# Optimization experiments

Hardware: AMD Instinct MI355X
Metric: run time of the kernel (lower is better)

The kernel has to match this reference:

```python
import jax, jax.numpy as jnp
import numpy as np


def setup_inputs() -> dict:
    key = jax.random.key(0)
    ks = jax.random.split(key, 5)
    B, Cin, Ch, H, W, K = 8, 64, 64, 128, 128, 3
    fan_in = (Cin + Ch) * K * K
    return {
        "x": jax.random.normal(ks[0], (B, Cin, H, W), jnp.float32),
        "prev_h": jax.random.normal(ks[1], (B, Ch, H, W), jnp.float32),
        "prev_c": jax.random.normal(ks[2], (B, Ch, H, W), jnp.float32),
        "W_gates": jax.random.normal(ks[3], (4 * Ch, Cin + Ch, K, K), jnp.float32) / np.sqrt(fan_in),
        "b_gates": jax.random.normal(ks[4], (4 * Ch,), jnp.float32) * 0.01,
    }


def reference(x, prev_h, prev_c, W_gates, b_gates):
    # ConvLSTM cell: conv over concat(input, prev_h) -> 4 gates -> gating.
    pad = W_gates.shape[-1] // 2
    stacked = jnp.concatenate([x, prev_h], axis=1)  # [B, Cin+Ch, H, W]
    gates = jax.lax.conv_general_dilated(
        stacked, W_gates,
        window_strides=(1, 1),
        padding=[(pad, pad), (pad, pad)],
        dimension_numbers=("NCHW", "OIHW", "NCHW"),
    ) + b_gates[None, :, None, None]  # [B, 4*Ch, H, W]
    in_gate, remember_gate, out_gate, cell_gate = jnp.split(gates, 4, axis=1)
    in_gate = jax.nn.sigmoid(in_gate)
    remember_gate = jax.nn.sigmoid(remember_gate)
    out_gate = jax.nn.sigmoid(out_gate)
    cell_gate = jnp.tanh(cell_gate)
    cell = in_gate * cell_gate + remember_gate * prev_c
    hidden = out_gate * jnp.tanh(cell)
    return (hidden, cell)
```

## Files before the change

### kernel.cpp

```cpp
#include <hip/hip_runtime.h>

typedef __attribute__((ext_vector_type(8))) short short8;
typedef __attribute__((ext_vector_type(4))) float float4v;

#define NPIX_HID 8388608
#define PST 136

__device__ __forceinline__ short f2bf(float f) {
    union { float f; unsigned u; } v; v.f = f;
    unsigned r = (v.u + 0x7FFFu + ((v.u >> 16) & 1u)) >> 16;
    return (short)r;
}

__device__ __forceinline__ float sigmoidf_(float v) { return 1.f / (1.f + __expf(-v)); }
__device__ __forceinline__ float tanhf_(float v)    { return 2.f / (1.f + __expf(-2.f * v)) - 1.f; }

__global__ void wprep(const float* __restrict__ W, short* __restrict__ A) {
    int tid = blockIdx.x * 256 + threadIdx.x;
    if (tid >= 9 * 16 * 256 * 8) return;
    int j   = tid & 7;
    int co  = (tid >> 3) & 255;
    int cig = (tid >> 11) & 15;
    int kk  = tid >> 15;
    int ci  = cig * 8 + j;
    A[tid] = f2bf(W[co * 1152 + ci * 9 + kk]);
}

__global__ __launch_bounds__(256, 2) void convlstm_main(
    const float* __restrict__ x, const float* __restrict__ ph,
    const float* __restrict__ pc, const short* __restrict__ aprep,
    const float* __restrict__ bg, float* __restrict__ out)
{
    __shared__ short Bs[4 * 66 * PST];

    const int tid  = threadIdx.x;
    const int lane = tid & 63;
    const int wave = tid >> 6;
    const int l15  = lane & 15;
    const int quad = lane >> 4;

    const int t  = blockIdx.x;
    const int x0 = (t & 1) * 64;
    const int y0 = ((t >> 1) & 63) * 2;
    const int b  = t >> 7;

    for (int i = tid; i < 4224; i += 256) {
        const int px  = i % 66;
        const int ro  = i / 66;
        const int oct = ro & 15;
        const int row = ro >> 4;
        const int ysrc = y0 + row - 1;
        const int xsrc = x0 + px - 1;
        short8 pk = {0,0,0,0,0,0,0,0};
        if ((unsigned)ysrc < 128u && (unsigned)xsrc < 128u) {
            const float* src = (oct < 8) ? x : ph;
            const float* sp = src + (((b * 64 + (oct & 7) * 8) * 128 + ysrc) * 128 + xsrc);
#pragma unroll
            for (int j = 0; j < 8; ++j) pk[j] = f2bf(sp[j * 16384]);
        }
        *(short8*)&Bs[(row * 66 + px) * PST + oct * 8] = pk;
    }
    __syncthreads();

    float4v acc[4][8];
#pragma unroll
    for (int mt = 0; mt < 4; ++mt)
#pragma unroll
        for (int nt = 0; nt < 8; ++nt)
            acc[mt][nt] = (float4v){0.f, 0.f, 0.f, 0.f};

    const int coff = (wave * 16 + l15) * 8;
    short8 afr[4];
    {
        const short* ab = aprep + quad * 2048;
#pragma unroll
        for (int mt = 0; mt < 4; ++mt)
            afr[mt] = *(const short8*)(ab + mt * 512 + coff);
    }

#pragma unroll 1
    for (int kt = 0; kt < 36; ++kt) {
        const int ktn = (kt < 35) ? kt + 1 : 35;
        short8 anx[4];
        const short* abn = aprep + ktn * 8192 + quad * 2048;
#pragma unroll
        for (int mt = 0; mt < 4; ++mt)
            anx[mt] = *(const short8*)(abn + mt * 512 + coff);

        const int kkk = kt >> 2;
        const int kc  = kt & 3;
        const int ky  = (kkk * 11) >> 5;
        const int kx  = kkk - ky * 3;
        const int kof = kc * 32 + quad * 8;

        short8 bfr[8];
#pragma unroll
        for (int nt = 0; nt < 8; ++nt) {
            const int rowh = ky + (nt >> 2);
            const int pxi  = kx + ((nt & 3) << 4) + l15;
            bfr[nt] = *(const short8*)&Bs[(rowh * 66 + pxi) * PST + kof];
        }
#pragma unroll
        for (int mt = 0; mt < 4; ++mt)
#pragma unroll
            for (int nt = 0; nt < 8; ++nt)
                acc[mt][nt] = __builtin_amdgcn_mfma_f32_16x16x32_bf16(
                    afr[mt], bfr[nt], acc[mt][nt], 0, 0, 0);
#pragma unroll
        for (int mt = 0; mt < 4; ++mt) afr[mt] = anx[mt];
    }

#pragma unroll
    for (int nt = 0; nt < 8; ++nt) {
        const int y  = y0 + (nt >> 2);
        const int px = x0 + ((nt & 3) << 4) + l15;
#pragma unroll
        for (int r = 0; r < 4; ++r) {
            const int c = wave * 16 + quad * 4 + r;
            const float gi = acc[0][nt][r] + bg[c];
            const float gf = acc[1][nt][r] + bg[64 + c];
            const float go = acc[2][nt][r] + bg[128 + c];
            const float gc = acc[3][nt][r] + bg[192 + c];
            const float ig = sigmoidf_(gi);
            const float fg = sigmoidf_(gf);
            const float og = sigmoidf_(go);
            const float cg = tanhf_(gc);
            const int idx = ((b * 64 + c) * 128 + y) * 128 + px;
            const float cell = ig * cg + fg * pc[idx];
            const float hid  = og * tanhf_(cell);
            out[idx] = hid;
            out[NPIX_HID + idx] = cell;
        }
    }
}

extern "C" void kernel_launch(void* const* d_in, const int* in_sizes, int n_in,
                              void* d_out, int out_size, void* d_ws, size_t ws_size,
                              hipStream_t stream) {
    const float* x  = (const float*)d_in[0];
    const float* ph = (const float*)d_in[1];
    const float* pc = (const float*)d_in[2];
    const float* W  = (const float*)d_in[3];
    const float* bg = (const float*)d_in[4];
    float* out = (float*)d_out;
    short* aprep = (short*)d_ws;

    wprep<<<1152, 256, 0, stream>>>(W, aprep);
    convlstm_main<<<1024, 256, 0, stream>>>(x, ph, pc, aprep, bg, out);
}
```

Baseline: 228.7 us.

## Switch to 32x32x16 MFMA with XOR-swizzled LDS and interleaved gate weight layout

The conv GEMM moves from 16x16x32 to 32x32x16 bf16 MFMA tiles. Each wave now covers half the channel rows and one spatial row, instead of a 16-channel slice across all pixels. Padded LDS rows are replaced with an XOR swizzle to avoid bank conflicts. Weights are reordered so all four gates for a channel land in one accumulator, and weight fragments are double-buffered with a manually unrolled K loop. This reduces LDS reads per MFMA and improves MFMA efficiency, at the cost of more complex indexing and possible register pressure under launch bounds of 2.

```diff
diff --git a/kernel.cpp b/kernel.cpp
--- a/kernel.cpp
+++ b/kernel.cpp
@@ -1,10 +1,9 @@
 #include <hip/hip_runtime.h>
 
 typedef __attribute__((ext_vector_type(8))) short short8;
-typedef __attribute__((ext_vector_type(4))) float float4v;
+typedef __attribute__((ext_vector_type(16))) float float16;
 
 #define NPIX_HID 8388608
-#define PST 136
 
 __device__ __forceinline__ short f2bf(float f) {
     union { float f; unsigned u; } v; v.f = f;
@@ -17,12 +16,15 @@
 
 __global__ void wprep(const float* __restrict__ W, short* __restrict__ A) {
     int tid = blockIdx.x * 256 + threadIdx.x;
-    if (tid >= 9 * 16 * 256 * 8) return;
+    if (tid >= 9 * 16 * 8 * 32 * 8) return;
     int j   = tid & 7;
-    int co  = (tid >> 3) & 255;
+    int r   = (tid >> 3) & 31;
+    int t   = (tid >> 8) & 7;
     int cig = (tid >> 11) & 15;
     int kk  = tid >> 15;
-    int ci  = cig * 8 + j;
+    int g = r >> 3, cl = r & 7;
+    int co = g * 64 + t * 8 + cl;
+    int ci = cig * 8 + j;
     A[tid] = f2bf(W[co * 1152 + ci * 9 + kk]);
 }
 
@@ -31,13 +33,15 @@
     const float* __restrict__ pc, const short* __restrict__ aprep,
     const float* __restrict__ bg, float* __restrict__ out)
 {
-    __shared__ short Bs[4 * 66 * PST];
+    __shared__ short Bs[4 * 66 * 128];
 
     const int tid  = threadIdx.x;
     const int lane = tid & 63;
     const int wave = tid >> 6;
-    const int l15  = lane & 15;
-    const int quad = lane >> 4;
+    const int l31  = lane & 31;
+    const int h    = lane >> 5;
+    const int mhalf = wave & 1;
+    const int nhalf = wave >> 1;
 
     const int t  = blockIdx.x;
     const int x0 = (t & 1) * 64;
@@ -58,78 +62,101 @@
 #pragma unroll
             for (int j = 0; j < 8; ++j) pk[j] = f2bf(sp[j * 16384]);
         }
-        *(short8*)&Bs[(row * 66 + px) * PST + oct * 8] = pk;
+        const int off16 = (row * 66 + px) * 16 + (oct ^ (px & 15));
+        *(short8*)&Bs[off16 * 8] = pk;
     }
     __syncthreads();
 
-    float4v acc[4][8];
+    float16 acc[4][2];
 #pragma unroll
     for (int mt = 0; mt < 4; ++mt)
 #pragma unroll
-        for (int nt = 0; nt < 8; ++nt)
-            acc[mt][nt] = (float4v){0.f, 0.f, 0.f, 0.f};
+        for (int nt = 0; nt < 2; ++nt)
+#pragma unroll
+            for (int e = 0; e < 16; ++e) acc[mt][nt][e] = 0.f;
 
-    const int coff = (wave * 16 + l15) * 8;
-    short8 afr[4];
-    {
-        const short* ab = aprep + quad * 2048;
+    const short* ap0 = aprep + h * 2048 + l31 * 8 + mhalf * 1024;
+    const short* ap1 = ap0 + 4096;
+
+    short8 abuf[2][2][4];
+#pragma unroll
+    for (int ks = 0; ks < 2; ++ks)
 #pragma unroll
         for (int mt = 0; mt < 4; ++mt)
-            afr[mt] = *(const short8*)(ab + mt * 512 + coff);
+            abuf[0][ks][mt] = *(const short8*)((ks ? ap1 : ap0) + mt * 256);
+
+    const int lB = l31;
+
+#define HALF_BODY(KT, P, ADV)                                                      \
+    {                                                                              \
+        const int kt  = (KT);                                                      \
+        const int kkk = kt >> 2, kc = kt & 3;                                      \
+        const int ky  = (kkk * 11) >> 5;                                           \
+        const int kx  = kkk - ky * 3;                                              \
+        if (ADV) { ap0 += 8192; ap1 += 8192;                                       \
+            _Pragma("unroll")                                                      \
+            for (int ks = 0; ks < 2; ++ks)                                         \
+                _Pragma("unroll")                                                  \
+                for (int mt = 0; mt < 4; ++mt)                                     \
+                    abuf[(P) ^ 1][ks][mt] =                                        \
+                        *(const short8*)((ks ? ap1 : ap0) + mt * 256);             \
+        }                                                                          \
+        const int pxb = kx + lB;                                                   \
+        const int q   = pxb & 15;                                                  \
+        const int rh  = ky + nhalf;                                                \
+        short8 bfr[2][2];                                                          \
+        _Pragma("unroll")                                                          \
+        for (int ks = 0; ks < 2; ++ks) {                                           \
+            const int gx = ((kc * 4 + ks * 2) | h) ^ q;                            \
+            _Pragma("unroll")                                                      \
+            for (int nt = 0; nt < 2; ++nt) {                                       \
+                const int off16 = (rh * 66 + nt * 32 + pxb) * 16 + gx;             \
+                bfr[ks][nt] = *(const short8*)&Bs[off16 * 8];                      \
+            }                                                                      \
+        }                                                                          \
+        _Pragma("unroll")                                                          \
+        for (int mt = 0; mt < 4; ++mt)                                             \
+            _Pragma("unroll")                                                      \
+            for (int nt = 0; nt < 2; ++nt) {                                       \
+                acc[mt][nt] = __builtin_amdgcn_mfma_f32_32x32x16_bf16(             \
+                    abuf[P][0][mt], bfr[0][nt], acc[mt][nt], 0, 0, 0);             \
+                acc[mt][nt] = __builtin_amdgcn_mfma_f32_32x32x16_bf16(             \
+                    abuf[P][1][mt], bfr[1][nt], acc[mt][nt], 0, 0, 0);             \
+            }                                                                      \
     }
 
 #pragma unroll 1
-    for (int kt = 0; kt < 36; ++kt) {
-        const int ktn = (kt < 35) ? kt + 1 : 35;
-        short8 anx[4];
-        const short* abn = aprep + ktn * 8192 + quad * 2048;
+    for (int it = 0; it < 18; ++it) {
+        const int kt0 = it * 2;
+        HALF_BODY(kt0, 0, 1)
+        HALF_BODY(kt0 + 1, 1, (it < 17))
+    }
+#undef HALF_BODY
+
+    const int yy = y0 + nhalf;
 #pragma unroll
-        for (int mt = 0; mt < 4; ++mt)
-            anx[mt] = *(const short8*)(abn + mt * 512 + coff);
-
-        const int kkk = kt >> 2;
-        const int kc  = kt & 3;
-        const int ky  = (kkk * 11) >> 5;
-        const int kx  = kkk - ky * 3;
-        const int kof = kc * 32 + quad * 8;
-
-        short8 bfr[8];
+    for (int mt = 0; mt < 4; ++mt) {
+        const int c0 = (mhalf * 4 + mt) * 8 + 4 * h;
 #pragma unroll
-        for (int nt = 0; nt < 8; ++nt) {
-            const int rowh = ky + (nt >> 2);
-            const int pxi  = kx + ((nt & 3) << 4) + l15;
-            bfr[nt] = *(const short8*)&Bs[(rowh * 66 + pxi) * PST + kof];
-        }
+        for (int nt = 0; nt < 2; ++nt) {
+            const int px = x0 + nt * 32 + l31;
 #pragma unroll
-        for (int mt = 0; mt < 4; ++mt)
-#pragma unroll
-            for (int nt = 0; nt < 8; ++nt)
-                acc[mt][nt] = __builtin_amdgcn_mfma_f32_16x16x32_bf16(
-                    afr[mt], bfr[nt], acc[mt][nt], 0, 0, 0);
-#pragma unroll
-        for (int mt = 0; mt < 4; ++mt) afr[mt] = anx[mt];
-    }
-
-#pragma unroll
-    for (int nt = 0; nt < 8; ++nt) {
-        const int y  = y0 + (nt >> 2);
-        const int px = x0 + ((nt & 3) << 4) + l15;
-#pragma unroll
-        for (int r = 0; r < 4; ++r) {
-            const int c = wave * 16 + quad * 4 + r;
-            const float gi = acc[0][nt][r] + bg[c];
-            const float gf = acc[1][nt][r] + bg[64 + c];
-            const float go = acc[2][nt][r] + bg[128 + c];
-            const float gc = acc[3][nt][r] + bg[192 + c];
-            const float ig = sigmoidf_(gi);
-            const float fg = sigmoidf_(gf);
-            const float og = sigmoidf_(go);
-            const float cg = tanhf_(gc);
-            const int idx = ((b * 64 + c) * 128 + y) * 128 + px;
-            const float cell = ig * cg + fg * pc[idx];
-            const float hid  = og * tanhf_(cell);
-            out[idx] = hid;
-            out[NPIX_HID + idx] = cell;
+            for (int a = 0; a < 4; ++a) {
+                const int c = c0 + a;
+                const float gi = acc[mt][nt][a]      + bg[c];
+                const float gf = acc[mt][nt][4 + a]  + bg[64 + c];
+                const float go = acc[mt][nt][8 + a]  + bg[128 + c];
+                const float gc = acc[mt][nt][12 + a] + bg[192 + c];
+                const float ig = sigmoidf_(gi);
+                const float fg = sigmoidf_(gf);
+                const float og = sigmoidf_(go);
+                const float cg = tanhf_(gc);
+                const int idx = ((b * 64 + c) * 128 + yy) * 128 + px;
+                const float cell = ig * cg + fg * pc[idx];
+                const float hid  = og * tanhf_(cell);
+                out[idx] = hid;
+                out[NPIX_HID + idx] = cell;
+            }
         }
     }
 }
```

New measurement: 235.0 us. 2.7% more time.
